# Optimization experiments

Measured on AMD Instinct MI355X. Metric: run time of the kernel, lower is better.

The kernel has to match this reference:

```python
import jax, jax.numpy as jnp
import numpy as np
import math

SI, VI = 128, 32
H_DIM = 32          # max(vi, vo) for q/k/v GVPs; max(vi, 0)=32 for weight_proj
HEADS = 4
N_ANCHORS = 32
S_H, V_H = SI // HEADS, VI // HEADS  # 32, 8


def _norm_no_nan(x, axis=-1, keepdims=False, eps=1e-8):
    return jnp.sqrt(jnp.maximum(jnp.sum(x * x, axis=axis, keepdims=keepdims), eps))


def _gvp_full(s, v, wh, ws_w, ws_b, wv, wsv_w, wsv_b):
    # GVP with activations=(silu, sigmoid), vector_gate=True, vo>0
    vt = jnp.swapaxes(v, -1, -2)                 # [..., 3, vi]
    vh = vt @ wh.T                               # [..., 3, h]
    vn = _norm_no_nan(vh, axis=-2)               # [..., h]
    s_out = jnp.concatenate([s, vn], -1) @ ws_w.T + ws_b   # [..., so]
    v_out = jnp.swapaxes(vh @ wv.T, -1, -2)      # [..., vo, 3]
    gate = jax.nn.sigmoid(s_out) @ wsv_w.T + wsv_b
    v_out = v_out * jax.nn.sigmoid(gate)[..., None]
    return jax.nn.silu(s_out), v_out


def _gvp_scalar(s, v, wh, ws_w, ws_b):
    # weight_proj: activations=(None, None), vo=0 -> scalar output only
    vt = jnp.swapaxes(v, -1, -2)
    vh = vt @ wh.T
    vn = _norm_no_nan(vh, axis=-2)
    return jnp.concatenate([s, vn], -1) @ ws_w.T + ws_b


def setup_inputs() -> dict:
    key = jax.random.key(0)
    ks = jax.random.split(key, 32)
    N, C = 8192, 16
    inp = {
        's': jax.random.normal(ks[0], (N, C, SI), jnp.float32),
        'v': jax.random.normal(ks[1], (N, C, VI, 3), jnp.float32),
    }

    def lin(k, out_d, in_d):
        return jax.random.normal(k, (out_d, in_d), jnp.float32) / math.sqrt(in_d)

    # weight_proj: GVP((128,32) -> (32,0)), h_dim = max(32,0) = 32
    inp['wp_wh'] = lin(ks[2], H_DIM, VI)
    inp['wp_ws_w'] = lin(ks[3], N_ANCHORS, H_DIM + SI)
    inp['wp_ws_b'] = jnp.zeros((N_ANCHORS,), jnp.float32)
    # to_q / to_k / to_v: GVP((128,32) -> (128,32)), h_dim = 32
    i = 4
    for p in ('q', 'k', 'vp'):
        inp[f'{p}_wh'] = lin(ks[i], H_DIM, VI); i += 1
        inp[f'{p}_ws_w'] = lin(ks[i], SI, H_DIM + SI); i += 1
        inp[f'{p}_ws_b'] = jnp.zeros((SI,), jnp.float32)
        inp[f'{p}_wv'] = lin(ks[i], VI, H_DIM); i += 1
        inp[f'{p}_wsv_w'] = lin(ks[i], VI, SI); i += 1
        inp[f'{p}_wsv_b'] = jnp.zeros((VI,), jnp.float32)
    return inp


def reference(s, v, wp_wh, wp_ws_w, wp_ws_b,
              q_wh, q_ws_w, q_ws_b, q_wv, q_wsv_w, q_wsv_b,
              k_wh, k_ws_w, k_ws_b, k_wv, k_wsv_w, k_wsv_b,
              vp_wh, vp_ws_w, vp_ws_b, vp_wv, vp_wsv_w, vp_wsv_b):
    N, C = s.shape[:2]
    H, r = HEADS, N_ANCHORS

    # Compress: softmax over nodes -> r anchors
    p_logits = _gvp_scalar(s, v, wp_wh, wp_ws_w, wp_ws_b)       # [N, C, r]
    p_weights = jax.nn.softmax(p_logits, axis=0)
    s_global = jnp.einsum('nca,ncs->acs', p_weights, s)          # [r, C, si]
    v_global = jnp.einsum('nca,ncvd->acvd', p_weights, v)        # [r, C, vi, 3]

    s_q, v_q = _gvp_full(s, v, q_wh, q_ws_w, q_ws_b, q_wv, q_wsv_w, q_wsv_b)
    s_k, v_k = _gvp_full(s_global, v_global, k_wh, k_ws_w, k_ws_b, k_wv, k_wsv_w, k_wsv_b)
    s_val, v_val = _gvp_full(s_global, v_global, vp_wh, vp_ws_w, vp_ws_b, vp_wv, vp_wsv_w, vp_wsv_b)

    # split heads
    qs = s_q.reshape(N, C, H, S_H); qv = v_q.reshape(N, C, H, V_H, 3)
    ks_ = s_k.reshape(r, C, H, S_H); kv = v_k.reshape(r, C, H, V_H, 3)
    vs = s_val.reshape(r, C, H, S_H); vv = v_val.reshape(r, C, H, V_H, 3)

    s_dot = jnp.einsum('nchs,rchs->nrch', qs, ks_)
    v_dot = jnp.einsum('nchvd,rchvd->nrch', qv, kv)
    energy = (s_dot + v_dot) / math.sqrt(S_H + V_H)
    alpha = jax.nn.softmax(energy, axis=1)                       # softmax over anchors r
    # dropout is identity at inference

    out_s = jnp.einsum('nrch,rchs->nchs', alpha, vs).reshape(N, C, SI)
    out_v = jnp.einsum('nrch,rchvd->nchvd', alpha, vv).reshape(N, C, VI, 3)
    return out_s, out_v
```

## Files before the change

### kernel.cpp

```cpp
#include <hip/hip_runtime.h>
#include <stdint.h>

typedef unsigned short ushort_t;
typedef __attribute__((ext_vector_type(8))) short short8;
typedef __attribute__((ext_vector_type(4))) float float4v;

static constexpr int N_=8192, C_=16;

static constexpr long OFF_LOGITS = 0;
static constexpr long OFF_PM  = 4194304;
static constexpr long OFF_PS  = 4210688;
static constexpr long OFF_M   = 4227072;
static constexpr long OFF_INV = 4227584;
static constexpr long OFF_SGL = 4228096;
static constexpr long OFF_VGL = 4293632;
static constexpr long OFF_KATT= 4342784;
static constexpr long OFF_VATT= 4408320;
static constexpr long OFF_WF  = 4473856;
static constexpr long WF_WHQ=0, WF_WHWP=1024, WF_KWH=2048, WF_KWS=3072, WF_KWV=23552,
  WF_KWSV=24576, WF_VWH=28672, WF_VWS=29696, WF_VWV=50176, WF_VWSV=51200,
  WF_B1=55296 , WF_BG=70656 ,
  WF_BV=72704 ;

static constexpr long VH_B   = 67108864;
static constexpr long AVN_B  = 92274688;
static constexpr long PART_B = 67108864;
static constexpr long PART_ROWSZ = 224;
static constexpr long PART_CHUNKSZ = 512*224;

__device__ __forceinline__ uint32_t f2bf(float f){
  uint32_t u = __float_as_uint(f);
  return (u + 0x7FFFu + ((u>>16)&1u)) >> 16;
}

__device__ __forceinline__ void split_bf(float f, short& hi, short& lo){
  uint32_t u = __float_as_uint(f);
  uint32_t h = (u + 0x7FFFu + ((u>>16)&1u)) >> 16;
  hi = (short)h;
  float fh = __uint_as_float(h << 16);
  float r = f - fh;
  uint32_t u2 = __float_as_uint(r);
  lo = (short)((u2 + 0x7FFFu + ((u2>>16)&1u)) >> 16);
}

__device__ __forceinline__ long katt_idx(int c, int h, int k, int r){
  int kt=k>>5, kk=k&31, nt=r>>4;
  int lane=((kk>>3)<<4)|(r&15), j=kk&7;
  return ((((long)(c*4+h)*2+kt)*2+nt)*64+lane)*8+j;
}
__device__ __forceinline__ long vatt_idx(int c, int h, int r, int n2){
  int nt=n2>>4;
  int lane=((r>>3)<<4)|(n2&15), j=r&7;
  return (((long)(c*4+h)*4+nt)*64+lane)*8+j;
}

__global__ void k0_prep(const float* __restrict__ wpwh, const float* __restrict__ wpws,
    const float* __restrict__ qwh, const float* __restrict__ qws, const float* __restrict__ qwv,
    const float* __restrict__ qwsv, const float* __restrict__ kwh, const float* __restrict__ kws,
    const float* __restrict__ kwv, const float* __restrict__ kwsv, const float* __restrict__ vwh,
    const float* __restrict__ vws, const float* __restrict__ vwv, const float* __restrict__ vwsv,
    float* __restrict__ wsf){
  int job=blockIdx.x, t=threadIdx.x;
  float* W = wsf + OFF_WF;
  auto tr=[&](const float* src, float* dst, int O, int J){
    for(int idx=t; idx<O*J; idx+=blockDim.x){int o=idx/J, j=idx-o*J; dst[j*O+o]=src[idx];}
  };
  switch(job){
    case 0: tr(qwh,  W+WF_WHQ, 32,32); break;
    case 1: tr(wpwh, W+WF_WHWP,32,32); break;
    case 2: tr(kwh,  W+WF_KWH, 32,32); break;
    case 3: tr(kws,  W+WF_KWS, 128,160); break;
    case 4: tr(kwv,  W+WF_KWV, 32,32); break;
    case 5: tr(kwsv, W+WF_KWSV,32,128); break;
    case 6: tr(vwh,  W+WF_VWH, 32,32); break;
    case 7: tr(vws,  W+WF_VWS, 128,160); break;
    case 8: tr(vwv,  W+WF_VWV, 32,32); break;
    case 9: tr(vwsv, W+WF_VWSV,32,128); break;
    case 10: {
      ushort_t* dst=(ushort_t*)(W+WF_B1);
      for(int idx=t; idx<30720; idx+=blockDim.x){
        int j=idx&7, lane=(idx>>3)&63, tn=idx>>9, nt=tn%10, kt=tn/10;
        int k=kt*32+((lane>>4)<<3)+j, n=nt*16+(lane&15);
        float val;
        if(k<128)       val = (n<128)? qws[n*160+k]            : wpws[(n-128)*160+k];
        else if(k<160)  val = (n<128)? qws[n*160+k]            : 0.f;
        else            val = (n<128)? 0.f                     : wpws[(n-128)*160+(k-32)];
        dst[idx]=(ushort_t)f2bf(val);
      } } break;
    case 11: {
      ushort_t* dst=(ushort_t*)(W+WF_BG);
      for(int idx=t; idx<4096; idx+=blockDim.x){
        int j=idx&7, lane=(idx>>3)&63, tn=idx>>9, nt=tn&1, kt=tn>>1;
        int k=kt*32+((lane>>4)<<3)+j, n=nt*16+(lane&15);
        dst[idx]=(ushort_t)f2bf(qwsv[n*128+k]);
      } } break;
    case 12: {
      ushort_t* dst=(ushort_t*)(W+WF_BV);
      for(int idx=t; idx<1024; idx+=blockDim.x){
        int j=idx&7, lane=(idx>>3)&63, nt=idx>>9;
        int k=((lane>>4)<<3)+j, n=nt*16+(lane&15);
        dst[idx]=(ushort_t)f2bf(qwv[n*32+k]);
      } } break;
  }
}

__global__ __launch_bounds__(256) void kA_vn(const float* __restrict__ v,
    const float* __restrict__ wsf, ushort_t* __restrict__ vh_s, ushort_t* __restrict__ avn_s){
  int t=threadIdx.x, wave=t>>6, lane=t&63;
  int h=lane&31, half=lane>>5;
  float wq[16], wp[16];
  #pragma unroll
  for(int ii=0;ii<16;ii++){
    wq[ii]=wsf[OFF_WF+WF_WHQ +(half*16+ii)*32+h];
    wp[ii]=wsf[OFF_WF+WF_WHWP+(half*16+ii)*32+h];
  }
  for(int it=0; it<16; it++){
    long inst = ((long)blockIdx.x*4 + wave)*16 + it;
    const float4* vp = (const float4*)(v + inst*96 + half*48);
    float va[48];
    #pragma unroll
    for(int q=0;q<12;q++){
      float4 x = vp[q];
      va[4*q]=x.x; va[4*q+1]=x.y; va[4*q+2]=x.z; va[4*q+3]=x.w;
    }
    float d0=0,d1=0,d2=0,e0=0,e1=0,e2=0;
    #pragma unroll
    for(int ii=0;ii<16;ii++){
      float v0=va[3*ii], v1=va[3*ii+1], v2=va[3*ii+2];
      d0+=v0*wq[ii]; d1+=v1*wq[ii]; d2+=v2*wq[ii];
      e0+=v0*wp[ii]; e1+=v1*wp[ii]; e2+=v2*wp[ii];
    }
    d0+=__shfl_xor(d0,32,64); d1+=__shfl_xor(d1,32,64); d2+=__shfl_xor(d2,32,64);
    e0+=__shfl_xor(e0,32,64); e1+=__shfl_xor(e1,32,64); e2+=__shfl_xor(e2,32,64);
    if(lane<32){
      float vn=sqrtf(fmaxf(d0*d0+d1*d1+d2*d2,1e-8f));
      float en=sqrtf(fmaxf(e0*e0+e1*e1+e2*e2,1e-8f));
      avn_s[inst*64+h]   =(ushort_t)f2bf(vn);
      avn_s[inst*64+32+h]=(ushort_t)f2bf(en);
      vh_s[(inst*3+0)*32+h]=(ushort_t)f2bf(d0);
      vh_s[(inst*3+1)*32+h]=(ushort_t)f2bf(d1);
      vh_s[(inst*3+2)*32+h]=(ushort_t)f2bf(d2);
    }
  }
}

__global__ __launch_bounds__(256) void kB_gemm(const float* __restrict__ s,
    float* __restrict__ wsf,
    const float* __restrict__ qwsb, const float* __restrict__ wpwsb,
    const float* __restrict__ qwsvb,
    ushort_t* __restrict__ qatt, const ushort_t* __restrict__ vh_s,
    const ushort_t* __restrict__ avn_s){
  __shared__ ushort_t sigl[4][16*136];
  __shared__ float    gsigl[4][16*33];
  int t=threadIdx.x, wave=t>>6, lane=t&63;
  int l15=lane&15, lq=lane>>4;
  long m0 = ((long)blockIdx.x*4 + wave)*16;
  const short8* B1 = (const short8*)(wsf + OFF_WF + WF_B1);
  const short8* BG = (const short8*)(wsf + OFF_WF + WF_BG);
  const short8* BV = (const short8*)(wsf + OFF_WF + WF_BV);
  float4v acc[10];
  #pragma unroll
  for(int i=0;i<10;i++) acc[i]=(float4v){0.f,0.f,0.f,0.f};
  #pragma unroll
  for(int kt=0;kt<4;kt++){
    const float* sp = s + (m0+l15)*128 + kt*32 + lq*8;
    float4 f0=*(const float4*)sp, f1=*(const float4*)(sp+4);
    short8 a;
    a[0]=(short)f2bf(f0.x); a[1]=(short)f2bf(f0.y); a[2]=(short)f2bf(f0.z); a[3]=(short)f2bf(f0.w);
    a[4]=(short)f2bf(f1.x); a[5]=(short)f2bf(f1.y); a[6]=(short)f2bf(f1.z); a[7]=(short)f2bf(f1.w);
    #pragma unroll
    for(int nt=0;nt<10;nt++)
      acc[nt]=__builtin_amdgcn_mfma_f32_16x16x32_bf16(a, B1[(kt*10+nt)*64+lane], acc[nt],0,0,0);
  }
  #pragma unroll
  for(int kt=4;kt<6;kt++){
    short8 a = *(const short8*)&avn_s[(m0+l15)*64 + (kt-4)*32 + lq*8];
    #pragma unroll
    for(int nt=0;nt<10;nt++)
      acc[nt]=__builtin_amdgcn_mfma_f32_16x16x32_bf16(a, B1[(kt*10+nt)*64+lane], acc[nt],0,0,0);
  }
  ushort_t* sl = sigl[wave]; float* gl = gsigl[wave];
  #pragma unroll
  for(int nt=0;nt<8;nt++){
    float b = qwsb[nt*16+l15];
    #pragma unroll
    for(int reg=0;reg<4;reg++){
      float x = acc[nt][reg] + b;
      float sg = 1.f/(1.f+__expf(-x));
      int row = lq*4+reg, col=nt*16+l15;
      long inst = m0+row;
      qatt[(inst*4 + (col>>5))*64 + (col&31)] = (ushort_t)f2bf(x*sg);
      sl[row*136+col] = (ushort_t)f2bf(sg);
    }
  }
  #pragma unroll
  for(int nt=8;nt<10;nt++){
    float b = wpwsb[(nt-8)*16+l15];
    #pragma unroll
    for(int reg=0;reg<4;reg++){
      long inst=m0+lq*4+reg;
      wsf[OFF_LOGITS + inst*32 + (nt-8)*16+l15] = acc[nt][reg]+b;
    }
  }
  __syncthreads();
  float4v g0=(float4v){0.f,0.f,0.f,0.f}, g1=g0;
  #pragma unroll
  for(int kt=0;kt<4;kt++){
    short8 a = *(const short8*)&sl[l15*136 + kt*32 + lq*8];
    g0=__builtin_amdgcn_mfma_f32_16x16x32_bf16(a, BG[(kt*2+0)*64+lane], g0,0,0,0);
    g1=__builtin_amdgcn_mfma_f32_16x16x32_bf16(a, BG[(kt*2+1)*64+lane], g1,0,0,0);
  }
  {
    float b0 = qwsvb[l15], b1 = qwsvb[16+l15];
    #pragma unroll
    for(int reg=0;reg<4;reg++){
      int row=lq*4+reg;
      gl[row*33 + l15]    = 1.f/(1.f+__expf(-(g0[reg]+b0)));
      gl[row*33 + 16+l15] = 1.f/(1.f+__expf(-(g1[reg]+b1)));
    }
  }
  __syncthreads();
  #pragma unroll
  for(int tt=0;tt<3;tt++){
    short8 a = *(const short8*)&vh_s[(m0*3 + tt*16 + l15)*32 + lq*8];
    float4v v0=(float4v){0.f,0.f,0.f,0.f}, v1=v0;
    v0=__builtin_amdgcn_mfma_f32_16x16x32_bf16(a, BV[0*64+lane], v0,0,0,0);
    v1=__builtin_amdgcn_mfma_f32_16x16x32_bf16(a, BV[1*64+lane], v1,0,0,0);
    #pragma unroll
    for(int nt2=0;nt2<2;nt2++){
      #pragma unroll
      for(int reg=0;reg<4;reg++){
        int lr = tt*16 + lq*4 + reg;
        int il = lr/3, d = lr - il*3;
        int o = nt2*16+l15;
        float val = (nt2? v1[reg] : v0[reg]) * gl[il*33+o];
        long inst = m0 + il;
        qatt[(inst*4 + (o>>3))*64 + 32 + (o&7)*3 + d] = (ushort_t)f2bf(val);
      }
    }
  }
}

__global__ __launch_bounds__(256) void k2a_stats(float* __restrict__ ws){
  int c = blockIdx.x; int chunk = blockIdx.y;
  int t=threadIdx.x; int i=t>>5, a=t&31;
  const float* L = ws + OFF_LOGITS;
  float m=-1e30f, sum=0.f;
  for(int k2=0;k2<32;k2++){
    int n = chunk*256 + k2*8 + i;
    float x = L[((long)n*16 + c)*32 + a];
    float mn = fmaxf(m,x);
    sum = sum*__expf(m-mn) + __expf(x-mn);
    m = mn;
  }
  __shared__ float sm[8][32], ss[8][32];
  sm[i][a]=m; ss[i][a]=sum;
  __syncthreads();
  if(t<32){
    float M=sm[0][t], S=ss[0][t];
    for(int q=1;q<8;q++){
      float mq=sm[q][t], sq_=ss[q][t];
      float mn=fmaxf(M,mq); S=S*__expf(M-mn)+sq_*__expf(mq-mn); M=mn;
    }
    ws[OFF_PM + (chunk*16+c)*32 + t]=M;
    ws[OFF_PS + (chunk*16+c)*32 + t]=S;
  }
}

__global__ __launch_bounds__(256) void k2b_merge(float* __restrict__ ws){
  int t = blockIdx.x*256 + threadIdx.x;
  if(t>=512) return;
  int c=t>>5, a=t&31;
  float M=-1e30f, S=0.f;
  for(int ch=0; ch<32; ch++){
    float mq=ws[OFF_PM+(ch*16+c)*32+a], sq_=ws[OFF_PS+(ch*16+c)*32+a];
    float mn=fmaxf(M,mq); S=S*__expf(M-mn)+sq_*__expf(mq-mn); M=mn;
  }
  ws[OFF_M + t]=M; ws[OFF_INV + t]=1.0f/S;
}

template<int NMT, bool ISV>
__device__ __forceinline__ void k3_body(const float* __restrict__ X, int dx0, int pb0,
    const float* __restrict__ L, float M0, float M1, float I0, float I1,
    int c, int nb0, int l15, int lq, float* __restrict__ partc){
  constexpr int XP = ISV ? 96 : 128;
  float4v acc[NMT][2];
  #pragma unroll
  for(int mi=0;mi<NMT;mi++){
    acc[mi][0]=(float4v){0.f,0.f,0.f,0.f};
    acc[mi][1]=(float4v){0.f,0.f,0.f,0.f};
  }
  #pragma unroll
  for(int kt=0;kt<4;kt++){
    int nb = nb0 + kt*32 + lq*8;
    short8 bh0, bl0, bh1, bl1;
    #pragma unroll
    for(int j=0;j<8;j++){
      long ro = ((long)(nb+j)*16 + c)*32;
      float w0 = __expf(L[ro + l15]      - M0) * I0;
      float w1 = __expf(L[ro + 16 + l15] - M1) * I1;
      short h_, lo_;
      split_bf(w0, h_, lo_); bh0[j]=h_; bl0[j]=lo_;
      split_bf(w1, h_, lo_); bh1[j]=h_; bl1[j]=lo_;
    }
    #pragma unroll
    for(int mi=0;mi<NMT;mi++){
      short8 ah, al_;
      #pragma unroll
      for(int j=0;j<8;j++){
        float f = X[((long)(nb+j)*16 + c)*XP + dx0 + mi*16 + l15];
        short h_, lo_;
        split_bf(f, h_, lo_); ah[j]=h_; al_[j]=lo_;
      }
      acc[mi][0]=__builtin_amdgcn_mfma_f32_16x16x32_bf16(ah,  bh0, acc[mi][0],0,0,0);
      acc[mi][0]=__builtin_amdgcn_mfma_f32_16x16x32_bf16(al_, bh0, acc[mi][0],0,0,0);
      acc[mi][0]=__builtin_amdgcn_mfma_f32_16x16x32_bf16(ah,  bl0, acc[mi][0],0,0,0);
      acc[mi][1]=__builtin_amdgcn_mfma_f32_16x16x32_bf16(ah,  bh1, acc[mi][1],0,0,0);
      acc[mi][1]=__builtin_amdgcn_mfma_f32_16x16x32_bf16(al_, bh1, acc[mi][1],0,0,0);
      acc[mi][1]=__builtin_amdgcn_mfma_f32_16x16x32_bf16(ah,  bl1, acc[mi][1],0,0,0);
    }
  }
  #pragma unroll
  for(int mi=0;mi<NMT;mi++){
    #pragma unroll
    for(int nt=0;nt<2;nt++){
      int a = nt*16 + l15;
      long row = (long)(a*16 + c);
      float4 val = make_float4(acc[mi][nt][0], acc[mi][nt][1], acc[mi][nt][2], acc[mi][nt][3]);
      *(float4*)&partc[row*PART_ROWSZ + pb0 + mi*16 + lq*4] = val;
    }
  }
}

__global__ __launch_bounds__(256) void k3_globals(const float* __restrict__ s,
    const float* __restrict__ v, const float* __restrict__ ws, float* __restrict__ part){
  int c = blockIdx.x & 15; int chunk = blockIdx.x >> 4;
  int t=threadIdx.x, wave=t>>6, lane=t&63;
  int l15=lane&15, lq=lane>>4;
  const float* L = ws + OFF_LOGITS;
  float M0 = ws[OFF_M   + c*32 + l15],      M1 = ws[OFF_M   + c*32 + 16 + l15];
  float I0 = ws[OFF_INV + c*32 + l15],      I1 = ws[OFF_INV + c*32 + 16 + l15];
  int nb0 = chunk*128;
  float* partc = part + (long)chunk*PART_CHUNKSZ;
  if(wave==0)      k3_body<4,false>(s, 0,  0,   L, M0,M1,I0,I1, c, nb0, l15, lq, partc);
  else if(wave==1) k3_body<4,false>(s, 64, 64,  L, M0,M1,I0,I1, c, nb0, l15, lq, partc);
  else if(wave==2) k3_body<3,true >(v, 0,  128, L, M0,M1,I0,I1, c, nb0, l15, lq, partc);
  else             k3_body<3,true >(v, 48, 176, L, M0,M1,I0,I1, c, nb0, l15, lq, partc);
}

__global__ __launch_bounds__(128) void k4_kvgvp(float* __restrict__ wsf,
    const float* __restrict__ part,
    const float* __restrict__ k_wsb, const float* __restrict__ k_wsvb,
    const float* __restrict__ v_wsb, const float* __restrict__ v_wsvb){
  int a = blockIdx.x >> 4, c = blockIdx.x & 15;
  int t=threadIdx.x, p=t>>6, lane=t&63;
  __shared__ __align__(16) float catw[2][160];
  __shared__ __align__(16) float vb2[96];
  __shared__ float vhb[2][96];
  __shared__ __align__(16) float sg[2][128];
  const float* W = wsf + OFF_WF;
  ushort_t* katt = (ushort_t*)(wsf + OFF_KATT);
  ushort_t* vatt = (ushort_t*)(wsf + OFF_VATT);
  long row = (long)a*16 + c;
  if(p==0){
    float4 accp = make_float4(0.f,0.f,0.f,0.f);
    if(lane<56){
      const float* pp = part + row*PART_ROWSZ + lane*4;
      #pragma unroll 8
      for(int ch=0; ch<64; ch++){
        float4 x = *(const float4*)(pp + (long)ch*PART_CHUNKSZ);
        accp.x+=x.x; accp.y+=x.y; accp.z+=x.z; accp.w+=x.w;
      }
    }
    if(lane<32)      *(float4*)&catw[0][lane*4]  = accp;
    else if(lane<56) *(float4*)&vb2[(lane-32)*4] = accp;
  }
  if(a==0){
    for(int idx=t; idx<1024; idx+=128){
      int h2=idx&3, kk=56+((idx>>2)&7), r=idx>>5;
      katt[katt_idx(c,h2,kk,r)]=0;
      vatt[vatt_idx(c,h2,r,kk)]=0;
    }
  }
  __syncthreads();
  if(p==1 && lane<32) *(float4*)&catw[1][lane*4] = *(const float4*)&catw[0][lane*4];
  const float* wht  = W + (p? WF_VWH  : WF_KWH);
  const float* wst  = W + (p? WF_VWS  : WF_KWS);
  const float* wvt  = W + (p? WF_VWV  : WF_KWV);
  const float* wsvt = W + (p? WF_VWSV : WF_KWSV);
  const float* bs   = p? v_wsb : k_wsb;
  const float* bsv  = p? v_wsvb : k_wsvb;
  float* cat = catw[p];
  float* vh  = vhb[p];
  float* sgp = sg[p];
  int h = lane&31, half = lane>>5;
  float d0=0.f,d1=0.f,d2=0.f;
  for(int i=half*16; i<half*16+16; i++){
    float w_=wht[i*32+h];
    d0+=vb2[3*i]*w_; d1+=vb2[3*i+1]*w_; d2+=vb2[3*i+2]*w_;
  }
  d0 += __shfl_xor(d0,32,64); d1 += __shfl_xor(d1,32,64); d2 += __shfl_xor(d2,32,64);
  if(lane<32){
    cat[128+h] = sqrtf(fmaxf(d0*d0+d1*d1+d2*d2, 1e-8f));
    vh[3*h]=d0; vh[3*h+1]=d1; vh[3*h+2]=d2;
  }
  __syncthreads();
  float a0=bs[lane], a1=bs[lane+64];
  for(int j=0;j<160;j+=4){
    float4 c4=*((float4*)&cat[j]);
    a0 += c4.x*wst[j*128+lane]      + c4.y*wst[(j+1)*128+lane]
        + c4.z*wst[(j+2)*128+lane]  + c4.w*wst[(j+3)*128+lane];
    a1 += c4.x*wst[j*128+64+lane]   + c4.y*wst[(j+1)*128+64+lane]
        + c4.z*wst[(j+2)*128+64+lane]+ c4.w*wst[(j+3)*128+64+lane];
  }
  float sig0=1.f/(1.f+__expf(-a0)), sig1=1.f/(1.f+__expf(-a1));
  float silu0=a0*sig0, silu1=a1*sig1;
  sgp[lane]=sig0; sgp[lane+64]=sig1;
  {
    int o=lane, hh2=o>>5, k=o&31;
    if(p==0) katt[katt_idx(c,hh2,k,a)] = (ushort_t)f2bf(silu0);
    else     vatt[vatt_idx(c,hh2,a,k)] = (ushort_t)f2bf(silu0);
  }
  {
    int o=lane+64, hh2=o>>5, k=o&31;
    if(p==0) katt[katt_idx(c,hh2,k,a)] = (ushort_t)f2bf(silu1);
    else     vatt[vatt_idx(c,hh2,a,k)] = (ushort_t)f2bf(silu1);
  }
  __syncthreads();
  float gacc=0.f;
  for(int o=half*64; o<half*64+64; o+=4){
    float4 s4_=*((float4*)&sgp[o]);
    gacc += s4_.x*wsvt[o*32+h]+s4_.y*wsvt[(o+1)*32+h]+s4_.z*wsvt[(o+2)*32+h]+s4_.w*wsvt[(o+3)*32+h];
  }
  gacc += __shfl_xor(gacc,32,64);
  float sgate = 1.f/(1.f+__expf(-(gacc + bsv[h])));
  float e0=0.f,e1=0.f,e2=0.f;
  for(int hh=half*16; hh<half*16+16; hh++){
    float w_=wvt[hh*32+h];
    e0+=vh[3*hh]*w_; e1+=vh[3*hh+1]*w_; e2+=vh[3*hh+2]*w_;
  }
  e0+=__shfl_xor(e0,32,64); e1+=__shfl_xor(e1,32,64); e2+=__shfl_xor(e2,32,64);
  if(lane<32){
    int hh2=lane>>3, oo=lane&7;
    float vals[3]={e0*sgate, e1*sgate, e2*sgate};
    #pragma unroll
    for(int d=0;d<3;d++){
      if(p==0) katt[katt_idx(c,hh2,32+oo*3+d,a)] = (ushort_t)f2bf(vals[d]);
      else     vatt[vatt_idx(c,hh2,a,32+oo*3+d)] = (ushort_t)f2bf(vals[d]);
    }
  }
}

__global__ __launch_bounds__(256) void k5_attn(const float* __restrict__ wsf, float* out){
  __shared__ ushort_t al[4][4*16*40];
  int t=threadIdx.x, wave=t>>6, lane=t&63;
  int l15=lane&15, lq=lane>>4;
  int c=blockIdx.y;
  long n0 = ((long)blockIdx.x*4+wave)*16;
  const ushort_t* qatt = (const ushort_t*)out;
  const short8* KA = (const short8*)(wsf + OFF_KATT);
  const short8* VA = (const short8*)(wsf + OFF_VATT);
  const float scale = 0.15811388300841897f;
  const short8 zero8 = {0,0,0,0,0,0,0,0};
  float4v e[4][2];
  #pragma unroll
  for(int h=0;h<4;h++){ e[h][0]=(float4v){0.f,0.f,0.f,0.f}; e[h][1]=e[h][0]; }
  #pragma unroll
  for(int h=0;h<4;h++){
    #pragma unroll
    for(int kt=0;kt<2;kt++){
      short8 a = *(const short8*)&qatt[(((n0+l15)*16 + c)*4 + h)*64 + kt*32 + lq*8];
      if(kt==1 && lq==3) a = zero8;
      e[h][0]=__builtin_amdgcn_mfma_f32_16x16x32_bf16(a, KA[(((c*4+h)*2+kt)*2+0)*64+lane], e[h][0],0,0,0);
      e[h][1]=__builtin_amdgcn_mfma_f32_16x16x32_bf16(a, KA[(((c*4+h)*2+kt)*2+1)*64+lane], e[h][1],0,0,0);
    }
  }
  ushort_t* alw = al[wave];
  #pragma unroll
  for(int h=0;h<4;h++){
    #pragma unroll
    for(int reg=0;reg<4;reg++){
      float a0=e[h][0][reg]*scale, a1=e[h][1][reg]*scale;
      float m=fmaxf(a0,a1);
      m=fmaxf(m,__shfl_xor(m,1,64)); m=fmaxf(m,__shfl_xor(m,2,64));
      m=fmaxf(m,__shfl_xor(m,4,64)); m=fmaxf(m,__shfl_xor(m,8,64));
      float p0=__expf(a0-m), p1=__expf(a1-m);
      float sum=p0+p1;
      sum+=__shfl_xor(sum,1,64); sum+=__shfl_xor(sum,2,64);
      sum+=__shfl_xor(sum,4,64); sum+=__shfl_xor(sum,8,64);
      float inv=1.f/sum;
      int row=lq*4+reg;
      alw[h*640 + row*40 + l15]      = (ushort_t)f2bf(p0*inv);
      alw[h*640 + row*40 + 16 + l15] = (ushort_t)f2bf(p1*inv);
    }
  }
  float* outv = out + 16777216;
  #pragma unroll
  for(int h=0;h<4;h++){
    short8 a = *(const short8*)&alw[h*640 + l15*40 + lq*8];
    #pragma unroll
    for(int nt=0;nt<4;nt++){
      float4v o_=(float4v){0.f,0.f,0.f,0.f};
      o_=__builtin_amdgcn_mfma_f32_16x16x32_bf16(a, VA[((c*4+h)*4+nt)*64+lane], o_,0,0,0);
      #pragma unroll
      for(int reg=0;reg<4;reg++){
        int n2=nt*16+l15, row=lq*4+reg;
        long inst=(n0+row)*16+c;
        float val=o_[reg];
        if(n2<32)      out[inst*128 + h*32+n2]=val;
        else if(n2<56) outv[inst*96 + h*24 + n2-32]=val;
      }
    }
  }
}

extern "C" void kernel_launch(void* const* d_in, const int* in_sizes, int n_in,
                              void* d_out, int out_size, void* d_ws, size_t ws_size,
                              hipStream_t stream){
  (void)in_sizes; (void)n_in; (void)out_size; (void)ws_size;
  const float* s = (const float*)d_in[0];
  const float* v = (const float*)d_in[1];
  float* wsf = (float*)d_ws;
  float* out = (float*)d_out;
  ushort_t* qatt  = (ushort_t*)d_out;
  ushort_t* vh_s  = (ushort_t*)((char*)d_out + VH_B);
  ushort_t* avn_s = (ushort_t*)((char*)d_out + AVN_B);
  float* part = (float*)((char*)d_out + PART_B);
  k0_prep<<<13,256,0,stream>>>(
      (const float*)d_in[2],(const float*)d_in[3],
      (const float*)d_in[5],(const float*)d_in[6],(const float*)d_in[8],(const float*)d_in[9],
      (const float*)d_in[11],(const float*)d_in[12],(const float*)d_in[14],(const float*)d_in[15],
      (const float*)d_in[17],(const float*)d_in[18],(const float*)d_in[20],(const float*)d_in[21], wsf);
  kA_vn<<<2048,256,0,stream>>>(v, wsf, vh_s, avn_s);
  kB_gemm<<<2048,256,0,stream>>>(s, wsf, (const float*)d_in[7], (const float*)d_in[4],
                                 (const float*)d_in[10], qatt, vh_s, avn_s);
  k2a_stats<<<dim3(16,32),256,0,stream>>>(wsf);
  k2b_merge<<<2,256,0,stream>>>(wsf);
  k3_globals<<<1024,256,0,stream>>>(s, v, wsf, part);
  k4_kvgvp<<<512,128,0,stream>>>(wsf, part, (const float*)d_in[13], (const float*)d_in[16],
                                 (const float*)d_in[19], (const float*)d_in[22]);
  k5_attn<<<dim3(128,16),256,0,stream>>>(wsf, out);
}
```

Before: 507.2 us.

## Fuse vector-norm projection kernel into GEMM kernel via LDS staging

Moves the per-instance vector projection and norm computation from a separate kernel into the start of the q-GVP GEMM kernel, storing the bf16 results in shared memory instead of global scratch. This removes a global write and read of the intermediate vh and norm buffers and one kernel launch. It adds LDS usage per block, which may reduce occupancy, and serializes the ALU projection work ahead of the MFMA work in each wave.

```diff
diff --git a/kernel.cpp b/kernel.cpp
--- a/kernel.cpp
+++ b/kernel.cpp
@@ -22,8 +22,6 @@
   WF_B1=55296 , WF_BG=70656 ,
   WF_BV=72704 ;
 
-static constexpr long VH_B   = 67108864;
-static constexpr long AVN_B  = 92274688;
 static constexpr long PART_B = 67108864;
 static constexpr long PART_ROWSZ = 224;
 static constexpr long PART_CHUNKSZ = 512*224;
@@ -104,60 +102,63 @@
   }
 }
 
-__global__ __launch_bounds__(256) void kA_vn(const float* __restrict__ v,
-    const float* __restrict__ wsf, ushort_t* __restrict__ vh_s, ushort_t* __restrict__ avn_s){
-  int t=threadIdx.x, wave=t>>6, lane=t&63;
-  int h=lane&31, half=lane>>5;
-  float wq[16], wp[16];
-  #pragma unroll
-  for(int ii=0;ii<16;ii++){
-    wq[ii]=wsf[OFF_WF+WF_WHQ +(half*16+ii)*32+h];
-    wp[ii]=wsf[OFF_WF+WF_WHWP+(half*16+ii)*32+h];
-  }
-  for(int it=0; it<16; it++){
-    long inst = ((long)blockIdx.x*4 + wave)*16 + it;
-    const float4* vp = (const float4*)(v + inst*96 + half*48);
-    float va[48];
-    #pragma unroll
-    for(int q=0;q<12;q++){
-      float4 x = vp[q];
-      va[4*q]=x.x; va[4*q+1]=x.y; va[4*q+2]=x.z; va[4*q+3]=x.w;
-    }
-    float d0=0,d1=0,d2=0,e0=0,e1=0,e2=0;
-    #pragma unroll
-    for(int ii=0;ii<16;ii++){
-      float v0=va[3*ii], v1=va[3*ii+1], v2=va[3*ii+2];
-      d0+=v0*wq[ii]; d1+=v1*wq[ii]; d2+=v2*wq[ii];
-      e0+=v0*wp[ii]; e1+=v1*wp[ii]; e2+=v2*wp[ii];
-    }
-    d0+=__shfl_xor(d0,32,64); d1+=__shfl_xor(d1,32,64); d2+=__shfl_xor(d2,32,64);
-    e0+=__shfl_xor(e0,32,64); e1+=__shfl_xor(e1,32,64); e2+=__shfl_xor(e2,32,64);
-    if(lane<32){
-      float vn=sqrtf(fmaxf(d0*d0+d1*d1+d2*d2,1e-8f));
-      float en=sqrtf(fmaxf(e0*e0+e1*e1+e2*e2,1e-8f));
-      avn_s[inst*64+h]   =(ushort_t)f2bf(vn);
-      avn_s[inst*64+32+h]=(ushort_t)f2bf(en);
-      vh_s[(inst*3+0)*32+h]=(ushort_t)f2bf(d0);
-      vh_s[(inst*3+1)*32+h]=(ushort_t)f2bf(d1);
-      vh_s[(inst*3+2)*32+h]=(ushort_t)f2bf(d2);
-    }
-  }
-}
-
 __global__ __launch_bounds__(256) void kB_gemm(const float* __restrict__ s,
+    const float* __restrict__ v,
     float* __restrict__ wsf,
     const float* __restrict__ qwsb, const float* __restrict__ wpwsb,
     const float* __restrict__ qwsvb,
-    ushort_t* __restrict__ qatt, const ushort_t* __restrict__ vh_s,
-    const ushort_t* __restrict__ avn_s){
+    ushort_t* __restrict__ qatt){
   __shared__ ushort_t sigl[4][16*136];
   __shared__ float    gsigl[4][16*33];
+  __shared__ ushort_t vhl[4][48*32];
+  __shared__ ushort_t avnl[4][16*64];
   int t=threadIdx.x, wave=t>>6, lane=t&63;
   int l15=lane&15, lq=lane>>4;
   long m0 = ((long)blockIdx.x*4 + wave)*16;
   const short8* B1 = (const short8*)(wsf + OFF_WF + WF_B1);
   const short8* BG = (const short8*)(wsf + OFF_WF + WF_BG);
   const short8* BV = (const short8*)(wsf + OFF_WF + WF_BV);
+  ushort_t* vhw  = vhl[wave];
+  ushort_t* avnw = avnl[wave];
+
+  {
+    int h=lane&31, half=lane>>5;
+    float wq[16], wp[16];
+    #pragma unroll
+    for(int ii=0;ii<16;ii++){
+      wq[ii]=wsf[OFF_WF+WF_WHQ +(half*16+ii)*32+h];
+      wp[ii]=wsf[OFF_WF+WF_WHWP+(half*16+ii)*32+h];
+    }
+    for(int it=0; it<16; it++){
+      long inst = m0 + it;
+      const float4* vp = (const float4*)(v + inst*96 + half*48);
+      float va[48];
+      #pragma unroll
+      for(int q=0;q<12;q++){
+        float4 x = vp[q];
+        va[4*q]=x.x; va[4*q+1]=x.y; va[4*q+2]=x.z; va[4*q+3]=x.w;
+      }
+      float d0=0,d1=0,d2=0,e0=0,e1=0,e2=0;
+      #pragma unroll
+      for(int ii=0;ii<16;ii++){
+        float v0=va[3*ii], v1=va[3*ii+1], v2=va[3*ii+2];
+        d0+=v0*wq[ii]; d1+=v1*wq[ii]; d2+=v2*wq[ii];
+        e0+=v0*wp[ii]; e1+=v1*wp[ii]; e2+=v2*wp[ii];
+      }
+      d0+=__shfl_xor(d0,32,64); d1+=__shfl_xor(d1,32,64); d2+=__shfl_xor(d2,32,64);
+      e0+=__shfl_xor(e0,32,64); e1+=__shfl_xor(e1,32,64); e2+=__shfl_xor(e2,32,64);
+      if(lane<32){
+        float vn=sqrtf(fmaxf(d0*d0+d1*d1+d2*d2,1e-8f));
+        float en=sqrtf(fmaxf(e0*e0+e1*e1+e2*e2,1e-8f));
+        avnw[it*64+h]    = (ushort_t)f2bf(vn);
+        avnw[it*64+32+h] = (ushort_t)f2bf(en);
+        vhw[(it*3+0)*32+h]=(ushort_t)f2bf(d0);
+        vhw[(it*3+1)*32+h]=(ushort_t)f2bf(d1);
+        vhw[(it*3+2)*32+h]=(ushort_t)f2bf(d2);
+      }
+    }
+  }
+
   float4v acc[10];
   #pragma unroll
   for(int i=0;i<10;i++) acc[i]=(float4v){0.f,0.f,0.f,0.f};
@@ -174,7 +175,7 @@
   }
   #pragma unroll
   for(int kt=4;kt<6;kt++){
-    short8 a = *(const short8*)&avn_s[(m0+l15)*64 + (kt-4)*32 + lq*8];
+    short8 a = *(const short8*)&avnw[l15*64 + (kt-4)*32 + lq*8];
     #pragma unroll
     for(int nt=0;nt<10;nt++)
       acc[nt]=__builtin_amdgcn_mfma_f32_16x16x32_bf16(a, B1[(kt*10+nt)*64+lane], acc[nt],0,0,0);
@@ -222,7 +223,7 @@
   __syncthreads();
   #pragma unroll
   for(int tt=0;tt<3;tt++){
-    short8 a = *(const short8*)&vh_s[(m0*3 + tt*16 + l15)*32 + lq*8];
+    short8 a = *(const short8*)&vhw[(tt*16 + l15)*32 + lq*8];
     float4v v0=(float4v){0.f,0.f,0.f,0.f}, v1=v0;
     v0=__builtin_amdgcn_mfma_f32_16x16x32_bf16(a, BV[0*64+lane], v0,0,0,0);
     v1=__builtin_amdgcn_mfma_f32_16x16x32_bf16(a, BV[1*64+lane], v1,0,0,0);
@@ -523,17 +524,14 @@
   float* wsf = (float*)d_ws;
   float* out = (float*)d_out;
   ushort_t* qatt  = (ushort_t*)d_out;
-  ushort_t* vh_s  = (ushort_t*)((char*)d_out + VH_B);
-  ushort_t* avn_s = (ushort_t*)((char*)d_out + AVN_B);
   float* part = (float*)((char*)d_out + PART_B);
   k0_prep<<<13,256,0,stream>>>(
       (const float*)d_in[2],(const float*)d_in[3],
       (const float*)d_in[5],(const float*)d_in[6],(const float*)d_in[8],(const float*)d_in[9],
       (const float*)d_in[11],(const float*)d_in[12],(const float*)d_in[14],(const float*)d_in[15],
       (const float*)d_in[17],(const float*)d_in[18],(const float*)d_in[20],(const float*)d_in[21], wsf);
-  kA_vn<<<2048,256,0,stream>>>(v, wsf, vh_s, avn_s);
-  kB_gemm<<<2048,256,0,stream>>>(s, wsf, (const float*)d_in[7], (const float*)d_in[4],
-                                 (const float*)d_in[10], qatt, vh_s, avn_s);
+  kB_gemm<<<2048,256,0,stream>>>(s, v, wsf, (const float*)d_in[7], (const float*)d_in[4],
+                                 (const float*)d_in[10], qatt);
   k2a_stats<<<dim3(16,32),256,0,stream>>>(wsf);
   k2b_merge<<<2,256,0,stream>>>(wsf);
   k3_globals<<<1024,256,0,stream>>>(s, v, wsf, part);
```

Measured after the change: 509.4 us. No clear change (+0.4%).
